# Performance work log

Measured on AMD Instinct MI355X. Metric: run time of the kernel, lower is better.

Reference implementation:

```python
import jax, jax.numpy as jnp
import numpy as np
import math

N_HEADS = 16
N_KV_HEADS = 4
HEAD_DIM = 64
BLOCK = 1024
ROPE_BASE = 10000.0


def rotate_half(x):
    x1, x2 = jnp.split(x, 2, axis=-1)
    return jnp.concatenate([-x2, x1], axis=-1)


def setup_inputs() -> dict:
    key = jax.random.key(0)
    ks = jax.random.split(key, 5)
    B, L, D = 1, 4096, 1024
    kv_dim = N_KV_HEADS * HEAD_DIM  # 256
    x = jax.random.normal(ks[0], (B, L, D), dtype=jnp.float32)
    wq = jax.random.normal(ks[1], (D, D), dtype=jnp.float32) * 0.02
    wk = jax.random.normal(ks[2], (kv_dim, D), dtype=jnp.float32) * 0.02
    wv = jax.random.normal(ks[3], (kv_dim, D), dtype=jnp.float32) * 0.02
    wo = jax.random.normal(ks[4], (D, D), dtype=jnp.float32) * 0.02
    return {"x": x, "wq": wq, "wk": wk, "wv": wv, "wo": wo}


def reference(x, wq, wk, wv, wo):
    B, L, D = x.shape
    # projections (nn.Linear: y = x @ W^T), split heads -> [B, H, L, hd]
    q = (x @ wq.T).reshape(B, L, N_HEADS, HEAD_DIM).transpose(0, 2, 1, 3)
    k = (x @ wk.T).reshape(B, L, N_KV_HEADS, HEAD_DIM).transpose(0, 2, 1, 3)
    v = (x @ wv.T).reshape(B, L, N_KV_HEADS, HEAD_DIM).transpose(0, 2, 1, 3)

    # RoPE (L <= original_max=8192 -> unscaled branch of YaRNRoPE)
    t = jnp.arange(L, dtype=jnp.float32)
    inv_freq = 1.0 / (ROPE_BASE ** (jnp.arange(0, HEAD_DIM, 2, dtype=jnp.float32) / HEAD_DIM))
    freqs = t[:, None] * inv_freq[None, :]            # [L, hd/2]
    emb = jnp.concatenate([freqs, freqs], axis=-1)    # [L, hd]
    cos, sin = jnp.cos(emb), jnp.sin(emb)             # broadcast over [B,H,L,hd]
    q = q * cos + rotate_half(q) * sin
    k = k * cos + rotate_half(k) * sin

    # GQA: repeat_interleave kv heads
    n_rep = N_HEADS // N_KV_HEADS
    k = jnp.repeat(k, n_rep, axis=1)
    v = jnp.repeat(v, n_rep, axis=1)

    # ring/blockwise attention (L % BLOCK == 0 -> no padding needed)
    scale = 1.0 / math.sqrt(HEAD_DIM)
    num_blocks = L // BLOCK
    outs = []
    kv_prev = None
    for i in range(num_blocks):
        s, e = i * BLOCK, (i + 1) * BLOCK
        qb = q[:, :, s:e, :]
        if kv_prev is None:
            kr, vr = k[:, :, :e, :], v[:, :, :e, :]
        else:
            # faithful to source: prev block is concatenated AND re-included in the slice
            kr = jnp.concatenate([kv_prev[0], k[:, :, s - BLOCK:e, :]], axis=2)
            vr = jnp.concatenate([kv_prev[1], v[:, :, s - BLOCK:e, :]], axis=2)
        scores = jnp.einsum('bhqd,bhkd->bhqk', qb, kr) * scale
        attn = jax.nn.softmax(scores, axis=-1)
        outs.append(jnp.einsum('bhqk,bhkd->bhqd', attn, vr))
        kv_prev = (k[:, :, s:e, :], v[:, :, s:e, :])

    out = jnp.concatenate(outs, axis=2)               # [B,H,L,hd]
    out = out.transpose(0, 2, 1, 3).reshape(B, L, D)  # [B,L,D]
    return (out @ wo.T, k, v)
```

## Files before the change

### kernel.cpp

```cpp
#include <hip/hip_runtime.h>
#include <hip/hip_bf16.h>
#include <stdint.h>

typedef float f32x4 __attribute__((ext_vector_type(4)));
typedef float f32x16 __attribute__((ext_vector_type(16)));
typedef short s16x8 __attribute__((ext_vector_type(8)));

static __device__ __forceinline__ f32x4 mfma16(s16x8 a, s16x8 b, f32x4 c) {
    return __builtin_amdgcn_mfma_f32_16x16x32_bf16(a, b, c, 0, 0, 0);
}
static __device__ __forceinline__ f32x16 mfma32(s16x8 a, s16x8 b, f32x16 c) {
    return __builtin_amdgcn_mfma_f32_32x32x16_bf16(a, b, c, 0, 0, 0);
}

__global__ __launch_bounds__(256) void k_costab(float* __restrict__ ct, float* __restrict__ st) {
    int i = blockIdx.x * 256 + threadIdx.x;
    int t = i >> 5, f = i & 31;
    float inv = powf(10000.0f, -(float)f / 32.0f);
    float a = (float)t * inv;
    ct[i] = cosf(a);
    st[i] = sinf(a);
}

__global__ __launch_bounds__(256) void k_convert(
        const float* __restrict__ x, const float* __restrict__ wq,
        const float* __restrict__ wk, const float* __restrict__ wv,
        const float* __restrict__ wo,
        __hip_bfloat16* __restrict__ xb, __hip_bfloat16* __restrict__ wb,
        __hip_bfloat16* __restrict__ wob) {
    size_t c = (size_t)blockIdx.x * 256 + threadIdx.x;
    if (c >= 1703936) return;
    size_t e = c * 4;
    const float* src;
    __hip_bfloat16* dst;
    if (e < 4194304) { src = x + e; dst = xb + e; }
    else if (e < 5242880) { src = wq + (e - 4194304); dst = wb + (e - 4194304); }
    else if (e < 5505024) { src = wk + (e - 5242880); dst = wb + (e - 4194304); }
    else if (e < 5767168) { src = wv + (e - 5505024); dst = wb + (e - 4194304); }
    else { src = wo + (e - 5767168); dst = wob + (e - 5767168); }
    float4 v = *(const float4*)src;
    ushort4 u;
    u.x = __bfloat16_as_ushort(__float2bfloat16(v.x));
    u.y = __bfloat16_as_ushort(__float2bfloat16(v.y));
    u.z = __bfloat16_as_ushort(__float2bfloat16(v.z));
    u.w = __bfloat16_as_ushort(__float2bfloat16(v.w));
    *(ushort4*)(void*)dst = u;
}

__global__ __launch_bounds__(256) void k_gemm_bt(
        const __hip_bfloat16* __restrict__ A, const __hip_bfloat16* __restrict__ B,
        float* __restrict__ C, int M, int N, int K) {
    __shared__ __hip_bfloat16 As[128][32];
    __shared__ __hip_bfloat16 Bs[128][32];
    int tid = threadIdx.x;
    int wave = tid >> 6, lane = tid & 63;
    int l15 = lane & 15, l4 = lane >> 4;
    int wr = (wave >> 1) * 64, wc = (wave & 1) * 64;
    int row0 = blockIdx.y * 128, col0 = blockIdx.x * 128;
    f32x4 acc[4][4] = {};
    int c0 = tid, c1 = tid + 256;
    int r0 = c0 >> 2, k0o = (c0 & 3) << 3;
    int r1 = c1 >> 2, k1o = (c1 & 3) << 3;
    for (int kb = 0; kb < K; kb += 32) {
        __syncthreads();
        *(s16x8*)(void*)&As[r0][k0o] = *(const s16x8*)(const void*)&A[(size_t)(row0 + r0) * K + kb + k0o];
        *(s16x8*)(void*)&As[r1][k1o] = *(const s16x8*)(const void*)&A[(size_t)(row0 + r1) * K + kb + k1o];
        *(s16x8*)(void*)&Bs[r0][k0o] = *(const s16x8*)(const void*)&B[(size_t)(col0 + r0) * K + kb + k0o];
        *(s16x8*)(void*)&Bs[r1][k1o] = *(const s16x8*)(const void*)&B[(size_t)(col0 + r1) * K + kb + k1o];
        __syncthreads();
        s16x8 af[4], bf[4];
#pragma unroll
        for (int m = 0; m < 4; m++) af[m] = *(const s16x8*)(const void*)&As[wr + m * 16 + l15][l4 * 8];
#pragma unroll
        for (int n = 0; n < 4; n++) bf[n] = *(const s16x8*)(const void*)&Bs[wc + n * 16 + l15][l4 * 8];
#pragma unroll
        for (int m = 0; m < 4; m++)
#pragma unroll
            for (int n = 0; n < 4; n++)
                acc[m][n] = mfma16(af[m], bf[n], acc[m][n]);
    }
#pragma unroll
    for (int m = 0; m < 4; m++)
#pragma unroll
        for (int n = 0; n < 4; n++)
#pragma unroll
            for (int r = 0; r < 4; r++)
                C[(size_t)(row0 + wr + m * 16 + l4 * 4 + r) * N + col0 + wc + n * 16 + l15] = acc[m][n][r];
}

__global__ __launch_bounds__(256) void k_rope(
        const float* __restrict__ raw, const float* __restrict__ ct, const float* __restrict__ st,
        __hip_bfloat16* __restrict__ qr, __hip_bfloat16* __restrict__ kr,
        float* __restrict__ outK, float* __restrict__ outV) {
    const float SC = 0.125f * 1.44269504088896340736f;
    int t = blockIdx.x;
    int tid = threadIdx.x;
    const float* r = raw + (size_t)t * 1536;
    for (int p = tid; p < 512; p += 256) {
        int head = p >> 5, f = p & 31;
        float a = r[head * 64 + f], b = r[head * 64 + f + 32];
        float c = ct[t * 32 + f], s = st[t * 32 + f];
        qr[(size_t)t * 1024 + head * 64 + f]      = __float2bfloat16((a * c - b * s) * SC);
        qr[(size_t)t * 1024 + head * 64 + f + 32] = __float2bfloat16((b * c + a * s) * SC);
    }
    if (tid < 128) {
        int kvh = tid >> 5, f = tid & 31;
        float a = r[1024 + kvh * 64 + f], b = r[1024 + kvh * 64 + f + 32];
        float c = ct[t * 32 + f], s = st[t * 32 + f];
        float ra = a * c - b * s, rb = b * c + a * s;
        kr[((size_t)kvh * 4096 + t) * 64 + f]      = __float2bfloat16(ra);
        kr[((size_t)kvh * 4096 + t) * 64 + f + 32] = __float2bfloat16(rb);
#pragma unroll
        for (int rep = 0; rep < 4; rep++) {
            outK[((size_t)(kvh * 4 + rep) * 4096 + t) * 64 + f]      = ra;
            outK[((size_t)(kvh * 4 + rep) * 4096 + t) * 64 + f + 32] = rb;
        }
    }
    {
        int kvh = tid >> 6, d = tid & 63;
        float v = r[1280 + tid];
#pragma unroll
        for (int rep = 0; rep < 4; rep++)
            outV[((size_t)(kvh * 4 + rep) * 4096 + t) * 64 + d] = v;
    }
}

__global__ __launch_bounds__(256) void k_vtrans(const float* __restrict__ raw,
                                                __hip_bfloat16* __restrict__ vt) {
    int tt = blockIdx.x, kvh = blockIdx.y;
    int tid = threadIdx.x;
    for (int w = tid; w < 512; w += 256) {
        int d = w >> 3, t8 = (w & 7) << 3;
        s16x8 p;
#pragma unroll
        for (int j = 0; j < 8; j++)
            p[j] = __bfloat16_as_short(
                __float2bfloat16(raw[(size_t)(tt * 64 + t8 + j) * 1536 + 1280 + kvh * 64 + d]));
        *(s16x8*)(void*)&vt[((size_t)kvh * 64 + d) * 4096 + tt * 64 + t8] = p;
    }
}

__global__ __launch_bounds__(256) void k_attn(
        const __hip_bfloat16* __restrict__ qr, const __hip_bfloat16* __restrict__ kr,
        const __hip_bfloat16* __restrict__ vt, __hip_bfloat16* __restrict__ ao) {
    const int qt = blockIdx.x, ib = blockIdx.y, h = blockIdx.z;
    const int kvh = h >> 2;
    const int tid = threadIdx.x, wave = tid >> 6, lane = tid & 63;
    const int l31 = lane & 31, hi = lane >> 5;
    const int q0 = ib * 1024 + qt * 128 + wave * 32;
    const __hip_bfloat16* Kh = kr + (size_t)kvh * 4096 * 64;
    const __hip_bfloat16* Vh = vt + (size_t)kvh * 64 * 4096;
    s16x8 qf[4];
#pragma unroll
    for (int dc = 0; dc < 4; dc++)
        qf[dc] = *(const s16x8*)(const void*)
            &qr[(size_t)(q0 + l31) * 1024 + h * 64 + dc * 16 + hi * 8];
    f32x16 oacc[2] = {};
    float mrow = -1e30f, lrow = 0.0f;
    const int kstart = (ib == 0) ? 0 : (ib - 1) * 1024;
    const int ntiles = (ib == 0) ? 16 : 32;
    const int nbias  = (ib == 0) ? 0 : 16;
    for (int t = 0; t < ntiles; t++) {
        const int k0 = kstart + t * 64;
        f32x16 s[2] = {};
#pragma unroll
        for (int dc = 0; dc < 4; dc++) {
#pragma unroll
            for (int ksub = 0; ksub < 2; ksub++) {
                s16x8 kf = *(const s16x8*)(const void*)
                    &Kh[(size_t)(k0 + ksub * 32 + l31) * 64 + dc * 16 + hi * 8];
                s[ksub] = mfma32(kf, qf[dc], s[ksub]);
            }
        }
        s16x8 vfr[4][2];
#pragma unroll
        for (int c = 0; c < 4; c++)
#pragma unroll
            for (int dh = 0; dh < 2; dh++)
                vfr[c][dh] = *(const s16x8*)(const void*)
                    &Vh[(size_t)(dh * 32 + l31) * 4096 + k0 + c * 16 + hi * 8];
        const float bias = (t < nbias) ? 1.0f : 0.0f;
        float mx = -1e30f;
#pragma unroll
        for (int ksub = 0; ksub < 2; ksub++)
#pragma unroll
            for (int r = 0; r < 16; r++) mx = fmaxf(mx, s[ksub][r]);
        mx = fmaxf(mx, __shfl_xor(mx, 32));
        mx += bias;
        if (!__all(mx <= mrow + 8.0f)) {
            float mnew = fmaxf(mrow, mx);
            float alpha = exp2f(mrow - mnew);
            lrow *= alpha;
            mrow = mnew;
#pragma unroll
            for (int rr = 0; rr < 16; rr++) {
                int qrow = (rr & 3) + 8 * (rr >> 2) + 4 * hi;
                float ar = __shfl(alpha, qrow);
                oacc[0][rr] *= ar;
                oacc[1][rr] *= ar;
            }
        }
        const float mb = mrow - bias;
        float sum = 0.0f;
        uint32_t w[2][4][2];
#pragma unroll
        for (int ksub = 0; ksub < 2; ksub++) {
            float pv[16];
#pragma unroll
            for (int r = 0; r < 16; r++) {
                pv[r] = exp2f(s[ksub][r] - mb);
                sum += pv[r];
            }
#pragma unroll
            for (int R = 0; R < 4; R++)
#pragma unroll
                for (int u = 0; u < 2; u++) {
                    uint32_t lo = (uint32_t)__bfloat16_as_ushort(__float2bfloat16(pv[4 * R + 2 * u]));
                    uint32_t hiw = (uint32_t)__bfloat16_as_ushort(__float2bfloat16(pv[4 * R + 2 * u + 1]));
                    w[ksub][R][u] = lo | (hiw << 16);
                }
        }
        sum += __shfl_xor(sum, 32);
        lrow += sum;
#pragma unroll
        for (int c = 0; c < 4; c++) {
            const int ksub = c >> 1, cb = c & 1;
            uint32_t send0 = hi ? w[ksub][2 * cb][0] : w[ksub][2 * cb + 1][0];
            uint32_t send1 = hi ? w[ksub][2 * cb][1] : w[ksub][2 * cb + 1][1];
            uint32_t own0  = hi ? w[ksub][2 * cb + 1][0] : w[ksub][2 * cb][0];
            uint32_t own1  = hi ? w[ksub][2 * cb + 1][1] : w[ksub][2 * cb][1];
            uint32_t rcv0 = (uint32_t)__shfl_xor((int)send0, 32);
            uint32_t rcv1 = (uint32_t)__shfl_xor((int)send1, 32);
            union { uint32_t u[4]; s16x8 v; } pu;
            pu.u[0] = hi ? rcv0 : own0;
            pu.u[1] = hi ? rcv1 : own1;
            pu.u[2] = hi ? own0 : rcv0;
            pu.u[3] = hi ? own1 : rcv1;
#pragma unroll
            for (int dh = 0; dh < 2; dh++)
                oacc[dh] = mfma32(pu.v, vfr[c][dh], oacc[dh]);
        }
    }
    float inv = 1.0f / lrow;
#pragma unroll
    for (int rr = 0; rr < 16; rr++) {
        int qrow = (rr & 3) + 8 * (rr >> 2) + 4 * hi;
        float iv = __shfl(inv, qrow);
#pragma unroll
        for (int dh = 0; dh < 2; dh++)
            ao[(size_t)(q0 + qrow) * 1024 + h * 64 + dh * 32 + l31] =
                __float2bfloat16(oacc[dh][rr] * iv);
    }
}

extern "C" void kernel_launch(void* const* d_in, const int* in_sizes, int n_in,
                              void* d_out, int out_size, void* d_ws, size_t ws_size,
                              hipStream_t stream) {
    const float* x  = (const float*)d_in[0];
    const float* wq = (const float*)d_in[1];
    const float* wk = (const float*)d_in[2];
    const float* wv = (const float*)d_in[3];
    const float* wo = (const float*)d_in[4];
    float* out0 = (float*)d_out;
    float* outK = out0 + 4194304;
    float* outV = out0 + 8388608;
    char* ws = (char*)d_ws;
    __hip_bfloat16* xb  = (__hip_bfloat16*)(ws + 0);
    __hip_bfloat16* wb  = (__hip_bfloat16*)(ws + 8388608);
    __hip_bfloat16* wob = (__hip_bfloat16*)(ws + 11534336);
    float* ct           = (float*)(ws + 13631488);
    float* st           = (float*)(ws + 14155776);
    float* raw          = (float*)(ws + 14680064);
    __hip_bfloat16* qr  = (__hip_bfloat16*)(ws + 39845888);
    __hip_bfloat16* kr  = (__hip_bfloat16*)(ws + 48234496);
    __hip_bfloat16* vt  = (__hip_bfloat16*)(ws + 50331648);
    __hip_bfloat16* ao  = (__hip_bfloat16*)(ws + 52428800);

    hipLaunchKernelGGL(k_costab, dim3(512), dim3(256), 0, stream, ct, st);
    hipLaunchKernelGGL(k_convert, dim3(6656), dim3(256), 0, stream, x, wq, wk, wv, wo, xb, wb, wob);
    hipLaunchKernelGGL(k_gemm_bt, dim3(12, 32), dim3(256), 0, stream, xb, wb, raw, 4096, 1536, 1024);
    hipLaunchKernelGGL(k_rope, dim3(4096), dim3(256), 0, stream, raw, ct, st, qr, kr, outK, outV);
    hipLaunchKernelGGL(k_vtrans, dim3(64, 4), dim3(256), 0, stream, raw, vt);
    hipLaunchKernelGGL(k_attn, dim3(8, 4, 16), dim3(256), 0, stream, qr, kr, vt, ao);
    hipLaunchKernelGGL(k_gemm_bt, dim3(8, 32), dim3(256), 0, stream, ao, wob, out0, 4096, 1024, 1024);
}
```

Before: 278.7 us.

## Double-buffer K fragments and use permlane32 swap in attention loop

Restructures the attention inner loop to prefetch the next tile's K fragments into a second register buffer while the current tile is computed, unrolling by two. It also replaces the shuffle-based half-wave exchange of P with the permlane32_swap builtin and turns the row max and row sum reductions into tree reductions. The aim is to hide global load latency and cut cross-lane shuffle cost, in exchange for higher register pressure, which may reduce occupancy.

New measurement: 305.9 us. 1.1x slower.

```diff
diff --git a/kernel.cpp b/kernel.cpp
--- a/kernel.cpp
+++ b/kernel.cpp
@@ -5,6 +5,7 @@
 typedef float f32x4 __attribute__((ext_vector_type(4)));
 typedef float f32x16 __attribute__((ext_vector_type(16)));
 typedef short s16x8 __attribute__((ext_vector_type(8)));
+typedef unsigned int u32x2 __attribute__((ext_vector_type(2)));
 
 static __device__ __forceinline__ f32x4 mfma16(s16x8 a, s16x8 b, f32x4 c) {
     return __builtin_amdgcn_mfma_f32_16x16x32_bf16(a, b, c, 0, 0, 0);
@@ -140,6 +141,99 @@
     }
 }
 
+__device__ __forceinline__ void load_k8(s16x8 (&kf)[8], const __hip_bfloat16* Kh,
+                                        int k0, int l31, int hi) {
+#pragma unroll
+    for (int dc = 0; dc < 4; dc++)
+#pragma unroll
+        for (int ksub = 0; ksub < 2; ksub++)
+            kf[dc * 2 + ksub] = *(const s16x8*)(const void*)
+                &Kh[(size_t)(k0 + ksub * 32 + l31) * 64 + dc * 16 + hi * 8];
+}
+__device__ __forceinline__ void load_v8(s16x8 (&vf)[8], const __hip_bfloat16* Vh,
+                                        int k0, int l31, int hi) {
+#pragma unroll
+    for (int c = 0; c < 4; c++)
+#pragma unroll
+        for (int dh = 0; dh < 2; dh++)
+            vf[c * 2 + dh] = *(const s16x8*)(const void*)
+                &Vh[(size_t)(dh * 32 + l31) * 4096 + k0 + c * 16 + hi * 8];
+}
+
+__device__ __forceinline__ void attn_tile(
+        const s16x8 (&kf)[8], const s16x8 (&qf)[4], const __hip_bfloat16* Vh,
+        int k0, int l31, int hi, float bias,
+        f32x16 (&oacc)[2], float& mrow, float& lrow) {
+    s16x8 vf[8];
+    load_v8(vf, Vh, k0, l31, hi);
+    f32x16 s[2] = {};
+#pragma unroll
+    for (int dc = 0; dc < 4; dc++) {
+        s[0] = mfma32(kf[dc * 2 + 0], qf[dc], s[0]);
+        s[1] = mfma32(kf[dc * 2 + 1], qf[dc], s[1]);
+    }
+    float m[16];
+#pragma unroll
+    for (int r = 0; r < 16; r++) m[r] = fmaxf(s[0][r], s[1][r]);
+#pragma unroll
+    for (int d = 8; d >= 1; d >>= 1)
+#pragma unroll
+        for (int r = 0; r < d; r++) m[r] = fmaxf(m[r], m[r + d]);
+    float mx = fmaxf(m[0], __shfl_xor(m[0], 32)) + bias;
+    if (!__all(mx <= mrow + 8.0f)) {
+        float mnew = fmaxf(mrow, mx);
+        float alpha = exp2f(mrow - mnew);
+        lrow *= alpha;
+        mrow = mnew;
+#pragma unroll
+        for (int rr = 0; rr < 16; rr++) {
+            int qrow = (rr & 3) + 8 * (rr >> 2) + 4 * hi;
+            float ar = __shfl(alpha, qrow);
+            oacc[0][rr] *= ar;
+            oacc[1][rr] *= ar;
+        }
+    }
+    const float mb = mrow - bias;
+    uint32_t w[2][4][2];
+    float pv0[16], pv1[16];
+#pragma unroll
+    for (int r = 0; r < 16; r++) pv0[r] = exp2f(s[0][r] - mb);
+#pragma unroll
+    for (int r = 0; r < 16; r++) pv1[r] = exp2f(s[1][r] - mb);
+#pragma unroll
+    for (int R = 0; R < 4; R++)
+#pragma unroll
+        for (int u = 0; u < 2; u++) {
+            uint32_t lo0 = (uint32_t)__bfloat16_as_ushort(__float2bfloat16(pv0[4 * R + 2 * u]));
+            uint32_t hi0 = (uint32_t)__bfloat16_as_ushort(__float2bfloat16(pv0[4 * R + 2 * u + 1]));
+            w[0][R][u] = lo0 | (hi0 << 16);
+            uint32_t lo1 = (uint32_t)__bfloat16_as_ushort(__float2bfloat16(pv1[4 * R + 2 * u]));
+            uint32_t hi1 = (uint32_t)__bfloat16_as_ushort(__float2bfloat16(pv1[4 * R + 2 * u + 1]));
+            w[1][R][u] = lo1 | (hi1 << 16);
+        }
+    float ps[16];
+#pragma unroll
+    for (int r = 0; r < 16; r++) ps[r] = pv0[r] + pv1[r];
+#pragma unroll
+    for (int d = 8; d >= 1; d >>= 1)
+#pragma unroll
+        for (int r = 0; r < d; r++) ps[r] += ps[r + d];
+    lrow += ps[0] + __shfl_xor(ps[0], 32);
+#pragma unroll
+    for (int c = 0; c < 4; c++) {
+        const int ksub = c >> 1, cb = c & 1;
+        u32x2 e0 = __builtin_amdgcn_permlane32_swap(w[ksub][2 * cb][0], w[ksub][2 * cb + 1][0], false, false);
+        u32x2 e1 = __builtin_amdgcn_permlane32_swap(w[ksub][2 * cb][1], w[ksub][2 * cb + 1][1], false, false);
+        union { uint32_t u[4]; s16x8 v; } pu;
+        pu.u[0] = e0[0];
+        pu.u[1] = e1[0];
+        pu.u[2] = e0[1];
+        pu.u[3] = e1[1];
+        oacc[0] = mfma32(pu.v, vf[c * 2 + 0], oacc[0]);
+        oacc[1] = mfma32(pu.v, vf[c * 2 + 1], oacc[1]);
+    }
+}
+
 __global__ __launch_bounds__(256) void k_attn(
         const __hip_bfloat16* __restrict__ qr, const __hip_bfloat16* __restrict__ kr,
         const __hip_bfloat16* __restrict__ vt, __hip_bfloat16* __restrict__ ao) {
@@ -160,86 +254,14 @@
     const int kstart = (ib == 0) ? 0 : (ib - 1) * 1024;
     const int ntiles = (ib == 0) ? 16 : 32;
     const int nbias  = (ib == 0) ? 0 : 16;
-    for (int t = 0; t < ntiles; t++) {
+    s16x8 kA[8], kB[8];
+    load_k8(kA, Kh, kstart, l31, hi);
+    for (int t = 0; t < ntiles; t += 2) {
         const int k0 = kstart + t * 64;
-        f32x16 s[2] = {};
-#pragma unroll
-        for (int dc = 0; dc < 4; dc++) {
-#pragma unroll
-            for (int ksub = 0; ksub < 2; ksub++) {
-                s16x8 kf = *(const s16x8*)(const void*)
-                    &Kh[(size_t)(k0 + ksub * 32 + l31) * 64 + dc * 16 + hi * 8];
-                s[ksub] = mfma32(kf, qf[dc], s[ksub]);
-            }
-        }
-        s16x8 vfr[4][2];
-#pragma unroll
-        for (int c = 0; c < 4; c++)
-#pragma unroll
-            for (int dh = 0; dh < 2; dh++)
-                vfr[c][dh] = *(const s16x8*)(const void*)
-                    &Vh[(size_t)(dh * 32 + l31) * 4096 + k0 + c * 16 + hi * 8];
-        const float bias = (t < nbias) ? 1.0f : 0.0f;
-        float mx = -1e30f;
-#pragma unroll
-        for (int ksub = 0; ksub < 2; ksub++)
-#pragma unroll
-            for (int r = 0; r < 16; r++) mx = fmaxf(mx, s[ksub][r]);
-        mx = fmaxf(mx, __shfl_xor(mx, 32));
-        mx += bias;
-        if (!__all(mx <= mrow + 8.0f)) {
-            float mnew = fmaxf(mrow, mx);
-            float alpha = exp2f(mrow - mnew);
-            lrow *= alpha;
-            mrow = mnew;
-#pragma unroll
-            for (int rr = 0; rr < 16; rr++) {
-                int qrow = (rr & 3) + 8 * (rr >> 2) + 4 * hi;
-                float ar = __shfl(alpha, qrow);
-                oacc[0][rr] *= ar;
-                oacc[1][rr] *= ar;
-            }
-        }
-        const float mb = mrow - bias;
-        float sum = 0.0f;
-        uint32_t w[2][4][2];
-#pragma unroll
-        for (int ksub = 0; ksub < 2; ksub++) {
-            float pv[16];
-#pragma unroll
-            for (int r = 0; r < 16; r++) {
-                pv[r] = exp2f(s[ksub][r] - mb);
-                sum += pv[r];
-            }
-#pragma unroll
-            for (int R = 0; R < 4; R++)
-#pragma unroll
-                for (int u = 0; u < 2; u++) {
-                    uint32_t lo = (uint32_t)__bfloat16_as_ushort(__float2bfloat16(pv[4 * R + 2 * u]));
-                    uint32_t hiw = (uint32_t)__bfloat16_as_ushort(__float2bfloat16(pv[4 * R + 2 * u + 1]));
-                    w[ksub][R][u] = lo | (hiw << 16);
-                }
-        }
-        sum += __shfl_xor(sum, 32);
-        lrow += sum;
-#pragma unroll
-        for (int c = 0; c < 4; c++) {
-            const int ksub = c >> 1, cb = c & 1;
-            uint32_t send0 = hi ? w[ksub][2 * cb][0] : w[ksub][2 * cb + 1][0];
-            uint32_t send1 = hi ? w[ksub][2 * cb][1] : w[ksub][2 * cb + 1][1];
-            uint32_t own0  = hi ? w[ksub][2 * cb + 1][0] : w[ksub][2 * cb][0];
-            uint32_t own1  = hi ? w[ksub][2 * cb + 1][1] : w[ksub][2 * cb][1];
-            uint32_t rcv0 = (uint32_t)__shfl_xor((int)send0, 32);
-            uint32_t rcv1 = (uint32_t)__shfl_xor((int)send1, 32);
-            union { uint32_t u[4]; s16x8 v; } pu;
-            pu.u[0] = hi ? rcv0 : own0;
-            pu.u[1] = hi ? rcv1 : own1;
-            pu.u[2] = hi ? own0 : rcv0;
-            pu.u[3] = hi ? own1 : rcv1;
-#pragma unroll
-            for (int dh = 0; dh < 2; dh++)
-                oacc[dh] = mfma32(pu.v, vfr[c][dh], oacc[dh]);
-        }
+        load_k8(kB, Kh, k0 + 64, l31, hi);
+        attn_tile(kA, qf, Vh, k0, l31, hi, (t < nbias) ? 1.0f : 0.0f, oacc, mrow, lrow);
+        if (t + 2 < ntiles) load_k8(kA, Kh, k0 + 128, l31, hi);
+        attn_tile(kB, qf, Vh, k0 + 64, l31, hi, (t + 1 < nbias) ? 1.0f : 0.0f, oacc, mrow, lrow);
     }
     float inv = 1.0f / lrow;
 #pragma unroll
```
